# Optimization experiments

Hardware: AMD Instinct MI355X
Metric: run time of the kernel (lower is better)

Reference implementation:

```python
import jax, jax.numpy as jnp
import numpy as np

CHEB_K = 2  # hops per support; stacked terms = 1 + 2*CHEB_K = 5


def setup_inputs() -> dict:
    key = jax.random.key(0)
    k1, k2, k3, k4, k5 = jax.random.split(key, 5)
    B, N, C, O, D = 16, 1024, 64, 64, 10
    return {
        "x": jax.random.normal(k1, (B, N, C), dtype=jnp.float32),
        "adj": jax.random.uniform(k2, (2, B, N, N), dtype=jnp.float32),
        "node_embedding": jax.random.normal(k3, (N, D), dtype=jnp.float32),
        "weights_pool": jax.random.normal(k4, (D, 2 * CHEB_K + 1, C, O), dtype=jnp.float32) * 0.1,
        "bias_pool": jax.random.normal(k5, (D, O), dtype=jnp.float32) * 0.1,
    }


def reference(x, adj, node_embedding, weights_pool, bias_pool):
    # k-hop graph aggregation over each of the 2 supports
    out = [x]
    for s in range(adj.shape[0]):
        a = adj[s]  # [B, N, N]
        x1 = x
        for _ in range(CHEB_K):
            x1 = jnp.einsum('bnm,bmc->bnc', a, x1)
            out.append(x1)
    x_g = jnp.stack(out, axis=2)  # [B, N, K, C] with K = 2*cheb_k+1 (already node-major)
    # per-node hypernetwork weights and bias from node embeddings
    weights = jnp.einsum('nd,dkio->nkio', node_embedding, weights_pool)  # [N, K, C, O]
    bias = node_embedding @ bias_pool  # [N, O]
    # per-node contraction over (K, C)
    return jnp.einsum('bnki,nkio->bno', x_g, weights) + bias
```

## Files before the change

kernel.cpp:

```cpp
#include <hip/hip_runtime.h>
#include <stdint.h>


typedef __attribute__((ext_vector_type(4))) float f32x4;
typedef __attribute__((ext_vector_type(2))) float f32x2;
typedef __attribute__((ext_vector_type(8))) short s16x8;
typedef __attribute__((ext_vector_type(8))) __bf16 bf16x8;

__device__ __forceinline__ unsigned short f2bf(float f) {
  union { float f; uint32_t u; } v; v.f = f;
  uint32_t r = v.u + 0x7FFFu + ((v.u >> 16) & 1u);
  return (unsigned short)(r >> 16);
}
__device__ __forceinline__ uint32_t pack2(float a, float b) {
  return (uint32_t)f2bf(a) | ((uint32_t)f2bf(b) << 16);
}

union FragU { s16x8 s; bf16x8 b; };

__device__ __forceinline__ void async_cp16(const void* g, void* l) {
  __builtin_amdgcn_global_load_lds(
      (const __attribute__((address_space(1))) void*)g,
      (__attribute__((address_space(3))) void*)l, 16, 0, 0);
}

#define WAITVM(n)                                                         \
  __builtin_amdgcn_s_waitcnt(((n) & 15) | ((((n) >> 4) & 3) << 14) |      \
                             (7 << 4) | (15 << 8))

__global__ void transpose_x(const float* __restrict__ x,
                            unsigned short* __restrict__ XT0) {
  __shared__ unsigned short tl[64][72];
  const int b = blockIdx.y, n0 = blockIdx.x * 64;
  const int tid = threadIdx.x;
  {
    const int c4 = (tid & 15) * 4;
#pragma unroll
    for (int i = 0; i < 4; ++i) {
      const int row = (tid >> 4) + i * 16;
      f32x4 v = *(const f32x4*)(x + ((size_t)(b * 1024 + n0 + row)) * 64 + c4);
      *(uint32_t*)&tl[row][c4]     = pack2(v[0], v[1]);
      *(uint32_t*)&tl[row][c4 + 2] = pack2(v[2], v[3]);
    }
  }
  __syncthreads();
  {
    const int c = tid >> 2;
    const int nch = (tid & 3) * 16;
    s16x8 s0, s1;
#pragma unroll
    for (int j = 0; j < 8; ++j) {
      s0[j] = (short)tl[nch + j][c];
      s1[j] = (short)tl[nch + 8 + j][c];
    }
    unsigned short* p = XT0 + (size_t)(b * 64 + c) * 1024 + n0 + nch;
    *(s16x8*)p = s0;
    *(s16x8*)(p + 8) = s1;
  }
}

__global__ void transpose_wp(const float* __restrict__ wp,
                             float* __restrict__ wpT) {
  __shared__ float tl[64][65];
  const int d = blockIdx.y;
  const int ki0 = blockIdx.x * 64;
  const int tid = threadIdx.x;
  const float* src = wp + (size_t)d * 20480;
  {
    const int o4 = (tid & 15) * 4;
#pragma unroll
    for (int i = 0; i < 4; ++i) {
      const int row = (tid >> 4) + i * 16;
      f32x4 v = *(const f32x4*)(src + (size_t)(ki0 + row) * 64 + o4);
      tl[row][o4] = v[0]; tl[row][o4 + 1] = v[1];
      tl[row][o4 + 2] = v[2]; tl[row][o4 + 3] = v[3];
    }
  }
  __syncthreads();
  {
    const int o = tid >> 2;
    const int kch = (tid & 3) * 16;
    float* dst = wpT + (size_t)d * 20480 + (size_t)o * 320 + ki0 + kch;
#pragma unroll
    for (int u = 0; u < 4; ++u) {
      f32x4 v = { tl[kch + 4 * u][o], tl[kch + 4 * u + 1][o],
                  tl[kch + 4 * u + 2][o], tl[kch + 4 * u + 3][o] };
      *(f32x4*)(dst + 4 * u) = v;
    }
  }
}

__global__ __launch_bounds__(256) void wgen(const float* __restrict__ wpT,
                                            const float* __restrict__ emb,
                                            unsigned short* __restrict__ WT) {
  const int idx = (blockIdx.x * 256 + threadIdx.x) * 2;
  const int n0 = blockIdx.y * 16;
  f32x2 wv[10];
#pragma unroll
  for (int d = 0; d < 10; ++d)
    wv[d] = *(const f32x2*)(wpT + (size_t)d * 20480 + idx);
#pragma unroll
  for (int g = 0; g < 16; ++g) {
    float a0 = 0.f, a1 = 0.f;
#pragma unroll
    for (int d = 0; d < 10; ++d) {
      const float e = emb[(n0 + g) * 10 + d];
      a0 += e * wv[d][0];
      a1 += e * wv[d][1];
    }
    *(uint32_t*)(WT + (size_t)(n0 + g) * 20480 + idx) = pack2(a0, a1);
  }
}

__global__ __launch_bounds__(256, 2) void hop_kernel(
    const float* __restrict__ adj, const unsigned short* __restrict__ XTin,
    float* __restrict__ Xout, unsigned short* __restrict__ XTout,
    int xt_shared, int write_xt, int rev) {
  __shared__ __align__(16) char smem[32768];
  const int bx = rev ? (15 - (int)blockIdx.x) : (int)blockIdx.x;
  const int slice = rev ? (31 - (int)blockIdx.y) : (int)blockIdx.y;
  const int b = slice & 15;
  const float* __restrict__ A = adj + (size_t)slice * (1024u * 1024u);
  const unsigned short* __restrict__ XT =
      XTin + (size_t)(xt_shared ? b : slice) * (64 * 1024);
  const int tid = threadIdx.x;
  const int wave = tid >> 6, lane = tid & 63;
  const int l15 = lane & 15, q = lane >> 4;
  const int rowbase = bx * 64;

  float* const Abase = (float*)smem + wave * 2048;

  const float* ag[4];
#pragma unroll
  for (int i = 0; i < 4; ++i) {
    const int wl = i * 4 + (lane >> 4);
    const int ch = (lane & 15) ^ (wl & 7);
    ag[i] = A + (size_t)(rowbase + wave * 16 + wl) * 1024 + ch * 4;
  }
  const unsigned short* bg[8];
#pragma unroll
  for (int t = 0; t < 4; ++t)
#pragma unroll
    for (int h = 0; h < 2; ++h)
      bg[t * 2 + h] = XT + (size_t)(t * 16 + l15) * 1024 + h * 32 + q * 8;

  f32x4 acc[4];
#pragma unroll
  for (int t = 0; t < 4; ++t) acc[t] = (f32x4){0.f, 0.f, 0.f, 0.f};

  s16x8 breg0[8], breg1[8];

  auto issueA = [&](int k0, int s) {
#pragma unroll
    for (int i = 0; i < 4; ++i)
      async_cp16(ag[i] + k0, Abase + s * 1024 + i * 256);
  };
  auto issueB = [&](int k0, s16x8 (&br)[8]) {
#pragma unroll
    for (int j = 0; j < 8; ++j) br[j] = *(const s16x8*)(bg[j] + k0);
  };
  auto compute = [&](int s, const s16x8 (&br)[8]) {
    const float* Ab = Abase + s * 1024;
    const int sw = l15 & 7;
#pragma unroll
    for (int h = 0; h < 2; ++h) {
      const int j0 = h * 8 + q * 2;
      f32x4 c0 = *(const f32x4*)(Ab + l15 * 64 + (j0 ^ sw) * 4);
      f32x4 c1 = *(const f32x4*)(Ab + l15 * 64 + ((j0 + 1) ^ sw) * 4);
      FragU af;
#pragma unroll
      for (int e = 0; e < 4; ++e) {
        af.s[e]     = (short)f2bf(c0[e]);
        af.s[e + 4] = (short)f2bf(c1[e]);
      }
#pragma unroll
      for (int t = 0; t < 4; ++t) {
        FragU bf; bf.s = br[t * 2 + h];
        acc[t] = __builtin_amdgcn_mfma_f32_16x16x32_bf16(af.b, bf.b, acc[t],
                                                         0, 0, 0);
      }
    }
  };

  issueA(0, 0);    issueB(0, breg0);
  issueA(64, 1);   issueB(64, breg1);
#pragma unroll 1
  for (int kt = 0; kt < 14; kt += 2) {
    WAITVM(12);
    compute(0, breg0);
    issueA((kt + 2) * 64, 0); issueB((kt + 2) * 64, breg0);
    WAITVM(12);
    compute(1, breg1);
    issueA((kt + 3) * 64, 1); issueB((kt + 3) * 64, breg1);
  }
  WAITVM(12);
  compute(0, breg0);
  WAITVM(0);
  compute(1, breg1);

  __syncthreads();
  float (*tile)[65] = (float(*)[65])smem;
#pragma unroll
  for (int t = 0; t < 4; ++t)
#pragma unroll
    for (int rr = 0; rr < 4; ++rr)
      tile[wave * 16 + q * 4 + rr][t * 16 + l15] = acc[t][rr];
  __syncthreads();

  {
    const int row = tid >> 2;
    const int cb = (tid & 3) * 16;
    float* __restrict__ outp = Xout + (size_t)slice * (1024 * 64) +
                               (size_t)(rowbase + row) * 64 + cb;
#pragma unroll
    for (int u = 0; u < 4; ++u) {
      f32x4 v = { tile[row][cb + 4 * u], tile[row][cb + 4 * u + 1],
                  tile[row][cb + 4 * u + 2], tile[row][cb + 4 * u + 3] };
      *(f32x4*)(outp + 4 * u) = v;
    }
  }
  if (write_xt) {
    const int c = tid >> 2;
    const int nch = (tid & 3) * 16;
    unsigned short* __restrict__ xtp = XTout + (size_t)slice * (64 * 1024) +
                                       (size_t)c * 1024 + rowbase + nch;
    s16x8 s0, s1;
#pragma unroll
    for (int j = 0; j < 8; ++j) {
      s0[j] = (short)f2bf(tile[nch + j][c]);
      s1[j] = (short)f2bf(tile[nch + 8 + j][c]);
    }
    *(s16x8*)xtp = s0;
    *(s16x8*)(xtp + 8) = s1;
  }
}

__global__ __launch_bounds__(256, 2) void final_kernel(
    const float* __restrict__ x, const float* __restrict__ X1,
    const float* __restrict__ X2, const unsigned short* __restrict__ WT,
    const float* __restrict__ emb, const float* __restrict__ bias_pool,
    float* __restrict__ out) {
  __shared__ unsigned short xg[2][16][328];
  const int tid = threadIdx.x;
  const int node_base = blockIdx.x * 2;

  for (int u = tid; u < 5120; u += 256) {
    const int nd = u / 2560;
    int rem = u - nd * 2560;
    const int bb = rem / 160;
    const int kiu = rem - bb * 160;
    const int ki = kiu * 2;
    const int k = ki >> 6;
    const int c = ki & 63;
    const int nn = node_base + nd;
    const float* src;
    if (k == 0) {
      src = x + ((size_t)bb * 1024 + nn) * 64 + c;
    } else {
      const float* arr = (k == 1 || k == 3) ? X1 : X2;
      const int s = (k >= 3) ? 1 : 0;
      src = arr + ((size_t)(s * 16 + bb) * 1024 + nn) * 64 + c;
    }
    f32x2 v = *(const f32x2*)src;
    *(uint32_t*)&xg[nd][bb][ki] = pack2(v[0], v[1]);
  }
  __syncthreads();

  const int wave = tid >> 6, lane = tid & 63;
  const int nd = wave >> 1, oh = wave & 1;
  const int l15 = lane & 15, q = lane >> 4;
  const int n = node_base + nd;
  f32x4 acc[2];
#pragma unroll
  for (int t = 0; t < 2; ++t) acc[t] = (f32x4){0.f, 0.f, 0.f, 0.f};

  const unsigned short* wt0 =
      WT + (size_t)n * 20480 + (size_t)l15 * 320 + q * 8;
#pragma unroll
  for (int ks = 0; ks < 10; ++ks) {
    const int k0 = ks * 32;
    FragU af;
    af.s = *(const s16x8*)&xg[nd][l15][k0 + q * 8];
#pragma unroll
    for (int tt = 0; tt < 2; ++tt) {
      const int t = oh * 2 + tt;
      FragU bf;
      bf.s = *(const s16x8*)(wt0 + (size_t)t * (16 * 320) + k0);
      acc[tt] = __builtin_amdgcn_mfma_f32_16x16x32_bf16(af.b, bf.b, acc[tt],
                                                        0, 0, 0);
    }
  }

#pragma unroll
  for (int tt = 0; tt < 2; ++tt) {
    const int o = (oh * 2 + tt) * 16 + l15;
    float bv = 0.f;
#pragma unroll
    for (int d = 0; d < 10; ++d)
      bv += emb[n * 10 + d] * bias_pool[d * 64 + o];
#pragma unroll
    for (int rr = 0; rr < 4; ++rr) {
      const int bb = q * 4 + rr;
      out[((size_t)bb * 1024 + n) * 64 + o] = acc[tt][rr] + bv;
    }
  }
}

extern "C" void kernel_launch(void* const* d_in, const int* in_sizes, int n_in,
                              void* d_out, int out_size, void* d_ws,
                              size_t ws_size, hipStream_t stream) {
  const float* x   = (const float*)d_in[0];
  const float* adj = (const float*)d_in[1];
  const float* emb = (const float*)d_in[2];
  const float* wp  = (const float*)d_in[3];
  const float* bp  = (const float*)d_in[4];
  float* out = (float*)d_out;

  char* ws = (char*)d_ws;
  unsigned short* XT0 = (unsigned short*)(ws);
  unsigned short* XT1 = (unsigned short*)(ws + ((size_t)2 << 20));
  float* X1  = (float*)(ws + ((size_t)6 << 20));
  float* X2  = (float*)(ws + ((size_t)14 << 20));
  float* wpT = (float*)(ws + ((size_t)22 << 20));
  unsigned short* WT = (unsigned short*)(ws + ((size_t)23 << 20));

  transpose_x<<<dim3(16, 16), dim3(256), 0, stream>>>(x, XT0);
  hop_kernel<<<dim3(16, 32), dim3(256), 0, stream>>>(adj, XT0, X1, XT1,
                                                     1, 1, 0);
  hop_kernel<<<dim3(16, 32), dim3(256), 0, stream>>>(adj, XT1, X2,
                                                     (unsigned short*)nullptr,
                                                     0, 0, 1);
  transpose_wp<<<dim3(5, 10), dim3(256), 0, stream>>>(wp, wpT);
  wgen<<<dim3(40, 64), dim3(256), 0, stream>>>(wpT, emb, WT);
  final_kernel<<<dim3(512), dim3(256), 0, stream>>>(x, X1, X2, WT, emb, bp,
                                                    out);
}
```

Measured before the change: 283.0 us.

## Fuse all stages into one persistent kernel with atomic grid barriers

Replaces the six kernel launches with a single 512-block kernel that runs the transposes, both hop passes, weight generation and the final contraction as phases separated by software grid barriers built on an atomic counter. Weight generation is moved to run after the second hop inside the same phase. The aim is to remove launch overhead and inter-kernel gaps. The risks are deadlock if all 512 blocks cannot be resident at once, barrier spin cost, and an extra memset launch to reset the counter.

After: 679.7 us. +140.2%, slower.

```diff
diff --git a/kernel.cpp b/kernel.cpp
--- a/kernel.cpp
+++ b/kernel.cpp
@@ -28,105 +28,24 @@
   __builtin_amdgcn_s_waitcnt(((n) & 15) | ((((n) >> 4) & 3) << 14) |      \
                              (7 << 4) | (15 << 8))
 
-__global__ void transpose_x(const float* __restrict__ x,
-                            unsigned short* __restrict__ XT0) {
-  __shared__ unsigned short tl[64][72];
-  const int b = blockIdx.y, n0 = blockIdx.x * 64;
-  const int tid = threadIdx.x;
-  {
-    const int c4 = (tid & 15) * 4;
-#pragma unroll
-    for (int i = 0; i < 4; ++i) {
-      const int row = (tid >> 4) + i * 16;
-      f32x4 v = *(const f32x4*)(x + ((size_t)(b * 1024 + n0 + row)) * 64 + c4);
-      *(uint32_t*)&tl[row][c4]     = pack2(v[0], v[1]);
-      *(uint32_t*)&tl[row][c4 + 2] = pack2(v[2], v[3]);
-    }
-  }
-  __syncthreads();
-  {
-    const int c = tid >> 2;
-    const int nch = (tid & 3) * 16;
-    s16x8 s0, s1;
-#pragma unroll
-    for (int j = 0; j < 8; ++j) {
-      s0[j] = (short)tl[nch + j][c];
-      s1[j] = (short)tl[nch + 8 + j][c];
-    }
-    unsigned short* p = XT0 + (size_t)(b * 64 + c) * 1024 + n0 + nch;
-    *(s16x8*)p = s0;
-    *(s16x8*)(p + 8) = s1;
-  }
-}
-
-__global__ void transpose_wp(const float* __restrict__ wp,
-                             float* __restrict__ wpT) {
-  __shared__ float tl[64][65];
-  const int d = blockIdx.y;
-  const int ki0 = blockIdx.x * 64;
-  const int tid = threadIdx.x;
-  const float* src = wp + (size_t)d * 20480;
-  {
-    const int o4 = (tid & 15) * 4;
-#pragma unroll
-    for (int i = 0; i < 4; ++i) {
-      const int row = (tid >> 4) + i * 16;
-      f32x4 v = *(const f32x4*)(src + (size_t)(ki0 + row) * 64 + o4);
-      tl[row][o4] = v[0]; tl[row][o4 + 1] = v[1];
-      tl[row][o4 + 2] = v[2]; tl[row][o4 + 3] = v[3];
-    }
-  }
-  __syncthreads();
-  {
-    const int o = tid >> 2;
-    const int kch = (tid & 3) * 16;
-    float* dst = wpT + (size_t)d * 20480 + (size_t)o * 320 + ki0 + kch;
-#pragma unroll
-    for (int u = 0; u < 4; ++u) {
-      f32x4 v = { tl[kch + 4 * u][o], tl[kch + 4 * u + 1][o],
-                  tl[kch + 4 * u + 2][o], tl[kch + 4 * u + 3][o] };
-      *(f32x4*)(dst + 4 * u) = v;
-    }
-  }
-}
-
-__global__ __launch_bounds__(256) void wgen(const float* __restrict__ wpT,
-                                            const float* __restrict__ emb,
-                                            unsigned short* __restrict__ WT) {
-  const int idx = (blockIdx.x * 256 + threadIdx.x) * 2;
-  const int n0 = blockIdx.y * 16;
-  f32x2 wv[10];
-#pragma unroll
-  for (int d = 0; d < 10; ++d)
-    wv[d] = *(const f32x2*)(wpT + (size_t)d * 20480 + idx);
-#pragma unroll
-  for (int g = 0; g < 16; ++g) {
-    float a0 = 0.f, a1 = 0.f;
-#pragma unroll
-    for (int d = 0; d < 10; ++d) {
-      const float e = emb[(n0 + g) * 10 + d];
-      a0 += e * wv[d][0];
-      a1 += e * wv[d][1];
-    }
-    *(uint32_t*)(WT + (size_t)(n0 + g) * 20480 + idx) = pack2(a0, a1);
-  }
-}
-
-__global__ __launch_bounds__(256, 2) void hop_kernel(
-    const float* __restrict__ adj, const unsigned short* __restrict__ XTin,
-    float* __restrict__ Xout, unsigned short* __restrict__ XTout,
-    int xt_shared, int write_xt, int rev) {
-  __shared__ __align__(16) char smem[32768];
-  const int bx = rev ? (15 - (int)blockIdx.x) : (int)blockIdx.x;
-  const int slice = rev ? (31 - (int)blockIdx.y) : (int)blockIdx.y;
-  const int b = slice & 15;
-  const float* __restrict__ A = adj + (size_t)slice * (1024u * 1024u);
-  const unsigned short* __restrict__ XT =
-      XTin + (size_t)(xt_shared ? b : slice) * (64 * 1024);
+__device__ __forceinline__ void gridbar(unsigned* cnt, unsigned target) {
+  __threadfence();
+  __syncthreads();
+  if (threadIdx.x == 0) {
+    atomicAdd(cnt, 1u);
+    while (atomicAdd(cnt, 0u) < target) __builtin_amdgcn_s_sleep(16);
+  }
+  __syncthreads();
+  __threadfence();
+}
+
+__device__ __forceinline__ void hop_body(
+    char* smem, const float* __restrict__ A,
+    const unsigned short* __restrict__ XT, float* __restrict__ Xout,
+    unsigned short* __restrict__ XTout, int write_xt, int rowbase) {
   const int tid = threadIdx.x;
   const int wave = tid >> 6, lane = tid & 63;
   const int l15 = lane & 15, q = lane >> 4;
-  const int rowbase = bx * 64;
 
   float* const Abase = (float*)smem + wave * 2048;
 
@@ -210,8 +129,7 @@
   {
     const int row = tid >> 2;
     const int cb = (tid & 3) * 16;
-    float* __restrict__ outp = Xout + (size_t)slice * (1024 * 64) +
-                               (size_t)(rowbase + row) * 64 + cb;
+    float* __restrict__ outp = Xout + (size_t)(rowbase + row) * 64 + cb;
 #pragma unroll
     for (int u = 0; u < 4; ++u) {
       f32x4 v = { tile[row][cb + 4 * u], tile[row][cb + 4 * u + 1],
@@ -222,8 +140,7 @@
   if (write_xt) {
     const int c = tid >> 2;
     const int nch = (tid & 3) * 16;
-    unsigned short* __restrict__ xtp = XTout + (size_t)slice * (64 * 1024) +
-                                       (size_t)c * 1024 + rowbase + nch;
+    unsigned short* __restrict__ xtp = XTout + (size_t)c * 1024 + rowbase + nch;
     s16x8 s0, s1;
 #pragma unroll
     for (int j = 0; j < 8; ++j) {
@@ -233,75 +150,176 @@
     *(s16x8*)xtp = s0;
     *(s16x8*)(xtp + 8) = s1;
   }
-}
-
-__global__ __launch_bounds__(256, 2) void final_kernel(
-    const float* __restrict__ x, const float* __restrict__ X1,
-    const float* __restrict__ X2, const unsigned short* __restrict__ WT,
-    const float* __restrict__ emb, const float* __restrict__ bias_pool,
-    float* __restrict__ out) {
-  __shared__ unsigned short xg[2][16][328];
+  __syncthreads();
+}
+
+__global__ __launch_bounds__(256, 2) void mega(
+    const float* __restrict__ x, const float* __restrict__ adj,
+    const float* __restrict__ emb, const float* __restrict__ wp,
+    const float* __restrict__ bp, float* __restrict__ out,
+    unsigned short* XT0, unsigned short* XT1, float* X1, float* X2,
+    float* wpT, unsigned short* WT, unsigned* cnt) {
+  __shared__ __align__(16) char smem[32768];
   const int tid = threadIdx.x;
-  const int node_base = blockIdx.x * 2;
-
-  for (int u = tid; u < 5120; u += 256) {
-    const int nd = u / 2560;
-    int rem = u - nd * 2560;
-    const int bb = rem / 160;
-    const int kiu = rem - bb * 160;
-    const int ki = kiu * 2;
-    const int k = ki >> 6;
-    const int c = ki & 63;
-    const int nn = node_base + nd;
-    const float* src;
-    if (k == 0) {
-      src = x + ((size_t)bb * 1024 + nn) * 64 + c;
-    } else {
-      const float* arr = (k == 1 || k == 3) ? X1 : X2;
-      const int s = (k >= 3) ? 1 : 0;
-      src = arr + ((size_t)(s * 16 + bb) * 1024 + nn) * 64 + c;
-    }
-    f32x2 v = *(const f32x2*)src;
-    *(uint32_t*)&xg[nd][bb][ki] = pack2(v[0], v[1]);
-  }
-  __syncthreads();
-
-  const int wave = tid >> 6, lane = tid & 63;
-  const int nd = wave >> 1, oh = wave & 1;
-  const int l15 = lane & 15, q = lane >> 4;
-  const int n = node_base + nd;
-  f32x4 acc[2];
-#pragma unroll
-  for (int t = 0; t < 2; ++t) acc[t] = (f32x4){0.f, 0.f, 0.f, 0.f};
-
-  const unsigned short* wt0 =
-      WT + (size_t)n * 20480 + (size_t)l15 * 320 + q * 8;
-#pragma unroll
-  for (int ks = 0; ks < 10; ++ks) {
-    const int k0 = ks * 32;
-    FragU af;
-    af.s = *(const s16x8*)&xg[nd][l15][k0 + q * 8];
+  const int bid = blockIdx.x;
+
+  if (bid < 256) {
+    const int b = bid >> 4, n0 = (bid & 15) * 64;
+    unsigned short (*tl)[72] = (unsigned short(*)[72])smem;
+    {
+      const int c4 = (tid & 15) * 4;
+#pragma unroll
+      for (int i = 0; i < 4; ++i) {
+        const int row = (tid >> 4) + i * 16;
+        f32x4 v =
+            *(const f32x4*)(x + ((size_t)(b * 1024 + n0 + row)) * 64 + c4);
+        *(uint32_t*)&tl[row][c4]     = pack2(v[0], v[1]);
+        *(uint32_t*)&tl[row][c4 + 2] = pack2(v[2], v[3]);
+      }
+    }
+    __syncthreads();
+    {
+      const int c = tid >> 2;
+      const int nch = (tid & 3) * 16;
+      s16x8 s0, s1;
+#pragma unroll
+      for (int j = 0; j < 8; ++j) {
+        s0[j] = (short)tl[nch + j][c];
+        s1[j] = (short)tl[nch + 8 + j][c];
+      }
+      unsigned short* p = XT0 + (size_t)(b * 64 + c) * 1024 + n0 + nch;
+      *(s16x8*)p = s0;
+      *(s16x8*)(p + 8) = s1;
+    }
+  } else if (bid < 306) {
+    const int jj = bid - 256;
+    const int d = jj / 5, ki0 = (jj % 5) * 64;
+    float (*tl)[65] = (float(*)[65])smem;
+    const float* src = wp + (size_t)d * 20480;
+    {
+      const int o4 = (tid & 15) * 4;
+#pragma unroll
+      for (int i = 0; i < 4; ++i) {
+        const int row = (tid >> 4) + i * 16;
+        f32x4 v = *(const f32x4*)(src + (size_t)(ki0 + row) * 64 + o4);
+        tl[row][o4] = v[0]; tl[row][o4 + 1] = v[1];
+        tl[row][o4 + 2] = v[2]; tl[row][o4 + 3] = v[3];
+      }
+    }
+    __syncthreads();
+    {
+      const int o = tid >> 2;
+      const int kch = (tid & 3) * 16;
+      float* dst = wpT + (size_t)d * 20480 + (size_t)o * 320 + ki0 + kch;
+#pragma unroll
+      for (int u = 0; u < 4; ++u) {
+        f32x4 v = { tl[kch + 4 * u][o], tl[kch + 4 * u + 1][o],
+                    tl[kch + 4 * u + 2][o], tl[kch + 4 * u + 3][o] };
+        *(f32x4*)(dst + 4 * u) = v;
+      }
+    }
+  }
+  gridbar(cnt, 512);
+
+  {
+    const int bx = bid & 15, slice = bid >> 4, b = slice & 15;
+    hop_body(smem, adj + (size_t)slice * 1048576,
+             XT0 + (size_t)b * 65536, X1 + (size_t)slice * 65536,
+             XT1 + (size_t)slice * 65536, 1, bx * 64);
+  }
+  gridbar(cnt, 1024);
+
+  {
+    const int job = 511 - bid;
+    const int bx = job & 15, slice = job >> 4;
+    hop_body(smem, adj + (size_t)slice * 1048576,
+             XT1 + (size_t)slice * 65536, X2 + (size_t)slice * 65536,
+             (unsigned short*)0, 0, bx * 64);
+    for (int j = bid; j < 2560; j += 512) {
+      const int jx = j % 40;
+      const int n0 = (j / 40) * 16;
+      const int idx = (jx * 256 + tid) * 2;
+      f32x2 wv[10];
+#pragma unroll
+      for (int d = 0; d < 10; ++d)
+        wv[d] = *(const f32x2*)(wpT + (size_t)d * 20480 + idx);
+#pragma unroll
+      for (int g = 0; g < 16; ++g) {
+        float a0 = 0.f, a1 = 0.f;
+#pragma unroll
+        for (int d = 0; d < 10; ++d) {
+          const float e = emb[(n0 + g) * 10 + d];
+          a0 += e * wv[d][0];
+          a1 += e * wv[d][1];
+        }
+        *(uint32_t*)(WT + (size_t)(n0 + g) * 20480 + idx) = pack2(a0, a1);
+      }
+    }
+  }
+  gridbar(cnt, 1536);
+
+  {
+    unsigned short (*xg)[16][328] = (unsigned short(*)[16][328])smem;
+    const int node_base = bid * 2;
+    for (int u = tid; u < 5120; u += 256) {
+      const int nd = u / 2560;
+      int rem = u - nd * 2560;
+      const int bb = rem / 160;
+      const int kiu = rem - bb * 160;
+      const int ki = kiu * 2;
+      const int k = ki >> 6;
+      const int c = ki & 63;
+      const int nn = node_base + nd;
+      const float* src;
+      if (k == 0) {
+        src = x + ((size_t)bb * 1024 + nn) * 64 + c;
+      } else {
+        const float* arr = (k == 1 || k == 3) ? X1 : X2;
+        const int s = (k >= 3) ? 1 : 0;
+        src = arr + ((size_t)(s * 16 + bb) * 1024 + nn) * 64 + c;
+      }
+      f32x2 v = *(const f32x2*)src;
+      *(uint32_t*)&xg[nd][bb][ki] = pack2(v[0], v[1]);
+    }
+    __syncthreads();
+
+    const int wave = tid >> 6, lane = tid & 63;
+    const int nd = wave >> 1, oh = wave & 1;
+    const int l15 = lane & 15, q = lane >> 4;
+    const int n = node_base + nd;
+    f32x4 acc[2];
+#pragma unroll
+    for (int t = 0; t < 2; ++t) acc[t] = (f32x4){0.f, 0.f, 0.f, 0.f};
+
+    const unsigned short* wt0 =
+        WT + (size_t)n * 20480 + (size_t)l15 * 320 + q * 8;
+#pragma unroll
+    for (int ks = 0; ks < 10; ++ks) {
+      const int k0 = ks * 32;
+      FragU af;
+      af.s = *(const s16x8*)&xg[nd][l15][k0 + q * 8];
+#pragma unroll
+      for (int tt = 0; tt < 2; ++tt) {
+        const int t = oh * 2 + tt;
+        FragU bf;
+        bf.s = *(const s16x8*)(wt0 + (size_t)t * (16 * 320) + k0);
+        acc[tt] = __builtin_amdgcn_mfma_f32_16x16x32_bf16(af.b, bf.b, acc[tt],
+                                                          0, 0, 0);
+      }
+    }
+
 #pragma unroll
     for (int tt = 0; tt < 2; ++tt) {
-      const int t = oh * 2 + tt;
-      FragU bf;
-      bf.s = *(const s16x8*)(wt0 + (size_t)t * (16 * 320) + k0);
-      acc[tt] = __builtin_amdgcn_mfma_f32_16x16x32_bf16(af.b, bf.b, acc[tt],
-                                                        0, 0, 0);
-    }
-  }
-
-#pragma unroll
-  for (int tt = 0; tt < 2; ++tt) {
-    const int o = (oh * 2 + tt) * 16 + l15;
-    float bv = 0.f;
-#pragma unroll
-    for (int d = 0; d < 10; ++d)
-      bv += emb[n * 10 + d] * bias_pool[d * 64 + o];
-#pragma unroll
-    for (int rr = 0; rr < 4; ++rr) {
-      const int bb = q * 4 + rr;
-      out[((size_t)bb * 1024 + n) * 64 + o] = acc[tt][rr] + bv;
+      const int o = (oh * 2 + tt) * 16 + l15;
+      float bv = 0.f;
+#pragma unroll
+      for (int d = 0; d < 10; ++d)
+        bv += emb[n * 10 + d] * bp[d * 64 + o];
+#pragma unroll
+      for (int rr = 0; rr < 4; ++rr) {
+        const int bb = q * 4 + rr;
+        out[((size_t)bb * 1024 + n) * 64 + o] = acc[tt][rr] + bv;
+      }
     }
   }
 }
@@ -323,15 +341,9 @@
   float* X2  = (float*)(ws + ((size_t)14 << 20));
   float* wpT = (float*)(ws + ((size_t)22 << 20));
   unsigned short* WT = (unsigned short*)(ws + ((size_t)23 << 20));
-
-  transpose_x<<<dim3(16, 16), dim3(256), 0, stream>>>(x, XT0);
-  hop_kernel<<<dim3(16, 32), dim3(256), 0, stream>>>(adj, XT0, X1, XT1,
-                                                     1, 1, 0);
-  hop_kernel<<<dim3(16, 32), dim3(256), 0, stream>>>(adj, XT1, X2,
-                                                     (unsigned short*)nullptr,
-                                                     0, 0, 1);
-  transpose_wp<<<dim3(5, 10), dim3(256), 0, stream>>>(wp, wpT);
-  wgen<<<dim3(40, 64), dim3(256), 0, stream>>>(wpT, emb, WT);
-  final_kernel<<<dim3(512), dim3(256), 0, stream>>>(x, X1, X2, WT, emb, bp,
-                                                    out);
-}
+  unsigned* cnt = (unsigned*)(ws + ((size_t)64 << 20));
+
+  hipMemsetAsync((void*)cnt, 0, 256, stream);
+  mega<<<dim3(512), dim3(256), 0, stream>>>(x, adj, emb, wp, bp, out, XT0,
+                                            XT1, X1, X2, wpT, WT, cnt);
+}
```
